# Kernel tuning notes

Hardware: AMD Instinct MI355X
Metric: run time of the kernel (lower is better)

Reference implementation:

```python
import jax, jax.numpy as jnp
import numpy as np

B, S, D_IN, H = 64, 512, 1024, 1024


def setup_inputs() -> dict:
    key = jax.random.key(0)
    ks = jax.random.split(key, 7)
    scale = 1.0 / np.sqrt(H)  # nn.LSTM init range ~ U(-1/sqrt(H), 1/sqrt(H))
    return {
        "x": jax.random.normal(ks[0], (B, S, D_IN), dtype=jnp.float32),
        "h0": jax.random.normal(ks[1], (1, B, H), dtype=jnp.float32),
        "c0": jax.random.normal(ks[2], (1, B, H), dtype=jnp.float32),
        "w_ih": jax.random.uniform(ks[3], (4 * H, D_IN), jnp.float32, -scale, scale),
        "w_hh": jax.random.uniform(ks[4], (4 * H, H), jnp.float32, -scale, scale),
        "b_ih": jax.random.uniform(ks[5], (4 * H,), jnp.float32, -scale, scale),
        "b_hh": jax.random.uniform(ks[6], (4 * H,), jnp.float32, -scale, scale),
    }


def reference(x, h0, c0, w_ih, w_hh, b_ih, b_hh):
    # Precompute the input projection for all timesteps: [B, S, 4H]
    x_proj = jnp.einsum("bsd,nd->bsn", x, w_ih)
    bias = b_ih + b_hh  # [4H]
    hdim = w_hh.shape[1]

    def step(carry, xp_t):
        h, c = carry  # [B, H] each
        gates = xp_t + h @ w_hh.T + bias  # [B, 4H], gate order i,f,g,o
        i = jax.nn.sigmoid(gates[:, 0 * hdim:1 * hdim])
        f = jax.nn.sigmoid(gates[:, 1 * hdim:2 * hdim])
        g = jnp.tanh(gates[:, 2 * hdim:3 * hdim])
        o = jax.nn.sigmoid(gates[:, 3 * hdim:4 * hdim])
        c_next = f * c + i * g
        h_next = o * jnp.tanh(c_next)
        return (h_next, c_next), None

    (h_n, _c_n), _ = jax.lax.scan(step, (h0[0], c0[0]), jnp.swapaxes(x_proj, 0, 1))
    # num_layers == 1 -> h_n_first is empty; final hidden state stacked on layer dim
    return h_n[None]  # [1, B, H]
```

## Files before the change

### kernel.cpp

```cpp
#include <hip/hip_runtime.h>

typedef short s8v __attribute__((ext_vector_type(8)));
typedef float f4v __attribute__((ext_vector_type(4)));
typedef unsigned short u16;

#define CH 128
#define NCH 4
#define NBLK 128

__device__ __forceinline__ u16 f2bf(float f) {
  unsigned u = __builtin_bit_cast(unsigned, f);
  u = (u + 0x7fffu + ((u >> 16) & 1u)) >> 16;
  return (u16)u;
}
__device__ __forceinline__ float bf2f(u16 h) {
  unsigned u = ((unsigned)h) << 16;
  return __builtin_bit_cast(float, u);
}

__global__ void k_cast(const float* __restrict__ x, const float* __restrict__ wih,
                       const float* __restrict__ whh, const float* __restrict__ bih,
                       const float* __restrict__ bhh, u16* __restrict__ xb,
                       u16* __restrict__ wihb, u16* __restrict__ whhb,
                       float* __restrict__ bias) {
  unsigned i = blockIdx.x * 256u + threadIdx.x;
  const unsigned NT = 8192u * 256u;
  for (unsigned j = i; j < 8388608u; j += NT) {
    float4 v = ((const float4*)x)[j];
    ushort4 o; o.x = f2bf(v.x); o.y = f2bf(v.y); o.z = f2bf(v.z); o.w = f2bf(v.w);
    ((ushort4*)xb)[j] = o;
  }
  if (i < 1048576u) {
    float4 v = ((const float4*)wih)[i];
    ushort4 o; o.x = f2bf(v.x); o.y = f2bf(v.y); o.z = f2bf(v.z); o.w = f2bf(v.w);
    ((ushort4*)wihb)[i] = o;
    float4 w = ((const float4*)whh)[i];
    ushort4 p; p.x = f2bf(w.x); p.y = f2bf(w.y); p.z = f2bf(w.z); p.w = f2bf(w.w);
    ((ushort4*)whhb)[i] = p;
  }
  if (i < 4096u) bias[i] = bih[i] + bhh[i];
}

__global__ __launch_bounds__(256, 2) void k_gemm(const u16* __restrict__ xb,
                                                 const u16* __restrict__ wihb,
                                                 u16* __restrict__ xpn, int s0) {
  __shared__ u16 lds[16384];
  const int t = threadIdx.x;
  const int bx = blockIdx.x;
  const int nt = bx & 31, mt = bx >> 5;
  const int lane = t & 63, w = t >> 6;
  const int wm = (w >> 1) * 64, wn = (w & 1) * 64;
  const int lr = lane & 15, lk = lane >> 4;
  f4v acc[4][4] = {};
  const size_t arow0 = (size_t)(mt * 512 + s0) * 1024;
  const size_t brow0 = (size_t)(nt * 128) * 1024;
  for (int k0 = 0; k0 < 1024; k0 += 64) {
    #pragma unroll
    for (int i = 0; i < 4; i++) {
      int f16 = i * 256 + t;
      int row = f16 >> 3;
      int colb = (f16 & 7) << 4;
      int dst = row * 128 + (colb ^ ((row & 7) << 4));
      s8v va = *(const s8v*)(xb + arow0 + (size_t)row * 1024 + k0 + (colb >> 1));
      *(s8v*)((char*)lds + dst) = va;
      s8v vb = *(const s8v*)(wihb + brow0 + (size_t)row * 1024 + k0 + (colb >> 1));
      *(s8v*)((char*)lds + 16384 + dst) = vb;
    }
    __syncthreads();
    #pragma unroll
    for (int ks = 0; ks < 2; ks++) {
      s8v af[4], bf[4];
      #pragma unroll
      for (int mi = 0; mi < 4; mi++) {
        int r = wm + mi * 16 + lr;
        int cb = (ks * 64 + lk * 16) ^ ((r & 7) << 4);
        af[mi] = *(const s8v*)((const char*)lds + r * 128 + cb);
      }
      #pragma unroll
      for (int ni = 0; ni < 4; ni++) {
        int r = wn + ni * 16 + lr;
        int cb = (ks * 64 + lk * 16) ^ ((r & 7) << 4);
        bf[ni] = *(const s8v*)((const char*)lds + 16384 + r * 128 + cb);
      }
      #pragma unroll
      for (int mi = 0; mi < 4; mi++)
        #pragma unroll
        for (int ni = 0; ni < 4; ni++)
          acc[mi][ni] = __builtin_amdgcn_mfma_f32_16x16x32_bf16(af[mi], bf[ni], acc[mi][ni], 0, 0, 0);
    }
    __syncthreads();
  }
  #pragma unroll
  for (int mi = 0; mi < 4; mi++)
    #pragma unroll
    for (int rr = 0; rr < 4; rr++) {
      int rl = wm + mi * 16 + lk * 4 + rr;
      size_t orow = ((size_t)mt * 128 + rl) * 4096;
      #pragma unroll
      for (int ni = 0; ni < 4; ni++) {
        int col = nt * 128 + wn + ni * 16 + lr;
        xpn[orow + col] = f2bf(acc[mi][ni][rr]);
      }
    }
}

__global__ void k_pack(const u16* __restrict__ xpn, u16* __restrict__ xpl) {
  const int t = threadIdx.x;
  const int bx = blockIdx.x;
  const int s = bx >> 4, ubg = bx & 15;
  const int g = t & 3, b = t >> 2;
  #pragma unroll
  for (int i = 0; i < 8; i++) {
    int ub = ubg * 8 + i;
    s8v v = *(const s8v*)(xpn + (size_t)(b * 128 + s) * 4096 + g * 1024 + ub * 8);
    *(s8v*)(xpl + (((size_t)s * 128 + ub) * 4 + g) * 512 + b * 8) = v;
  }
}

__device__ __forceinline__ void gbar2(unsigned* flags, unsigned ep) {
  __syncthreads();
  if (threadIdx.x < 64) {
    if (threadIdx.x == 0)
      __hip_atomic_store(flags + (size_t)blockIdx.x * 16, ep,
                         __ATOMIC_RELAXED, __HIP_MEMORY_SCOPE_AGENT);
    const int l = threadIdx.x;
    for (;;) {
      unsigned a = __hip_atomic_load(flags + l * 16,        __ATOMIC_RELAXED, __HIP_MEMORY_SCOPE_AGENT);
      unsigned b = __hip_atomic_load(flags + (l + 64) * 16, __ATOMIC_RELAXED, __HIP_MEMORY_SCOPE_AGENT);
      if (__all(a >= ep && b >= ep)) break;
    }
  }
  __syncthreads();
}

__global__ __launch_bounds__(256, 1) void k_rec(
    const u16* __restrict__ whhb, const u16* __restrict__ xpl,
    const float* __restrict__ bias, const float* __restrict__ h0,
    const float* __restrict__ c0, float* __restrict__ cst,
    u16* __restrict__ hbuf, float* __restrict__ out,
    unsigned* flags, int chunk) {
  const int t = threadIdx.x, bid = blockIdx.x;
  const int lane = t & 63, w = t >> 6, lr = lane & 15, lk = lane >> 4;
  s8v breg[2][32];
  #pragma unroll
  for (int nt = 0; nt < 2; nt++) {
    int grow = (lr >> 2) * 1024 + bid * 8 + nt * 4 + (lr & 3);
    const u16* wp = whhb + (size_t)grow * 1024 + lk * 8;
    #pragma unroll
    for (int ks = 0; ks < 32; ks++) breg[nt][ks] = *(const s8v*)(wp + ks * 32);
  }
  const int m = t >> 2, up = t & 3;
  const int gu0 = bid * 8 + up * 2;
  const float2 bi  = *(const float2*)(bias + gu0);
  const float2 bff = *(const float2*)(bias + 1024 + gu0);
  const float2 bgg = *(const float2*)(bias + 2048 + gu0);
  const float2 bo  = *(const float2*)(bias + 3072 + gu0);
  float2 c;
  unsigned barn = 0;
  if (chunk == 0) {
    c = *(const float2*)(c0 + m * 1024 + gu0);
    float2 hv = *(const float2*)(h0 + m * 1024 + gu0);
    unsigned hw = (unsigned)f2bf(hv.x) | ((unsigned)f2bf(hv.y) << 16);
    asm volatile("global_store_dword %0, %1, off sc0 sc1"
                 :: "v"(hbuf + m * 1024 + gu0), "v"(hw) : "memory");
    asm volatile("s_waitcnt vmcnt(0)" ::: "memory");
    barn++; gbar2(flags, barn);
  } else {
    c = *(const float2*)(cst + m * 1024 + gu0);
  }
  __shared__ float gl[2048];
  int cur = 0;
  for (int tl = 0; tl < CH; tl++) {
    const u16* xb_ = xpl + ((size_t)tl * 128 + bid) * 2048;
    unsigned xpr[4];
    #pragma unroll
    for (int g = 0; g < 4; g++)
      asm volatile("global_load_dword %0, %1, off"
                   : "=v"(xpr[g]) : "v"(xb_ + g * 512 + m * 8 + up * 2) : "memory");
    const u16* ap = hbuf + cur * 65536 + (w * 16 + lr) * 1024 + lk * 8;
    s8v af[32];
    #pragma unroll
    for (int ks = 0; ks < 32; ks++)
      asm volatile("global_load_dwordx4 %0, %1, off sc0 sc1"
                   : "=v"(af[ks]) : "v"(ap + ks * 32) : "memory");
    f4v acc0 = {0.f, 0.f, 0.f, 0.f}, acc1 = {0.f, 0.f, 0.f, 0.f};
    asm volatile("s_waitcnt vmcnt(16)" ::: "memory");
    __builtin_amdgcn_sched_barrier(0);
    #pragma unroll
    for (int ks = 0; ks < 16; ks++) {
      acc0 = __builtin_amdgcn_mfma_f32_16x16x32_bf16(af[ks], breg[0][ks], acc0, 0, 0, 0);
      acc1 = __builtin_amdgcn_mfma_f32_16x16x32_bf16(af[ks], breg[1][ks], acc1, 0, 0, 0);
    }
    asm volatile("s_waitcnt vmcnt(0)" ::: "memory");
    __builtin_amdgcn_sched_barrier(0);
    #pragma unroll
    for (int ks = 16; ks < 32; ks++) {
      acc0 = __builtin_amdgcn_mfma_f32_16x16x32_bf16(af[ks], breg[0][ks], acc0, 0, 0, 0);
      acc1 = __builtin_amdgcn_mfma_f32_16x16x32_bf16(af[ks], breg[1][ks], acc1, 0, 0, 0);
    }
    #pragma unroll
    for (int r = 0; r < 4; r++) {
      int mrow = w * 16 + lk * 4 + r;
      gl[mrow * 32 + ((lr & 3)) * 4 + (lr >> 2)] = acc0[r];
      gl[mrow * 32 + (4 + (lr & 3)) * 4 + (lr >> 2)] = acc1[r];
    }
    __syncthreads();
    float4 q0 = *(const float4*)(gl + m * 32 + up * 8);
    float4 q1 = *(const float4*)(gl + m * 32 + up * 8 + 4);
    float pi0 = q0.x + bf2f((u16)(xpr[0] & 0xffff)) + bi.x;
    float pf0 = q0.y + bf2f((u16)(xpr[1] & 0xffff)) + bff.x;
    float pg0 = q0.z + bf2f((u16)(xpr[2] & 0xffff)) + bgg.x;
    float po0 = q0.w + bf2f((u16)(xpr[3] & 0xffff)) + bo.x;
    float pi1 = q1.x + bf2f((u16)(xpr[0] >> 16)) + bi.y;
    float pf1 = q1.y + bf2f((u16)(xpr[1] >> 16)) + bff.y;
    float pg1 = q1.z + bf2f((u16)(xpr[2] >> 16)) + bgg.y;
    float po1 = q1.w + bf2f((u16)(xpr[3] >> 16)) + bo.y;
    float i0 = 1.f / (1.f + __expf(-pi0)), i1 = 1.f / (1.f + __expf(-pi1));
    float f0 = 1.f / (1.f + __expf(-pf0)), f1 = 1.f / (1.f + __expf(-pf1));
    float g0 = 1.f - 2.f / (__expf(2.f * pg0) + 1.f), g1 = 1.f - 2.f / (__expf(2.f * pg1) + 1.f);
    float o0 = 1.f / (1.f + __expf(-po0)), o1 = 1.f / (1.f + __expf(-po1));
    c.x = f0 * c.x + i0 * g0;
    c.y = f1 * c.y + i1 * g1;
    float hv0 = o0 * (1.f - 2.f / (__expf(2.f * c.x) + 1.f));
    float hv1 = o1 * (1.f - 2.f / (__expf(2.f * c.y) + 1.f));
    int nxt = cur ^ 1;
    unsigned hw = (unsigned)f2bf(hv0) | ((unsigned)f2bf(hv1) << 16);
    asm volatile("global_store_dword %0, %1, off sc0 sc1"
                 :: "v"(hbuf + nxt * 65536 + m * 1024 + gu0), "v"(hw) : "memory");
    cur = nxt;
    if (tl < CH - 1) {
      asm volatile("s_waitcnt vmcnt(0)" ::: "memory");
      barn++; gbar2(flags, barn);
    } else {
      if (chunk == NCH - 1) *(float2*)(out + m * 1024 + gu0) = make_float2(hv0, hv1);
      else *(float2*)(cst + m * 1024 + gu0) = c;
    }
  }
}

extern "C" void kernel_launch(void* const* d_in, const int* in_sizes, int n_in,
                              void* d_out, int out_size, void* d_ws, size_t ws_size,
                              hipStream_t stream) {
  const float* x   = (const float*)d_in[0];
  const float* h0  = (const float*)d_in[1];
  const float* c0  = (const float*)d_in[2];
  const float* wih = (const float*)d_in[3];
  const float* whh = (const float*)d_in[4];
  const float* bih = (const float*)d_in[5];
  const float* bhh = (const float*)d_in[6];
  float* out = (float*)d_out;
  char* ws = (char*)d_ws;
  u16* xb     = (u16*)(ws);
  u16* wihb   = (u16*)(ws + 67108864);
  u16* whhb   = (u16*)(ws + 75497472);
  float* bias = (float*)(ws + 83886080);
  u16* hbuf   = (u16*)(ws + 83902464);
  float* cst  = (float*)(ws + 84164608);
  unsigned* flags = (unsigned*)(ws + 84426752);
  u16* xpn    = (u16*)(ws + 84443136);
  u16* xpl    = (u16*)(ws + 151552000);
  (void)in_sizes; (void)n_in; (void)out_size; (void)ws_size;

  hipLaunchKernelGGL(k_cast, dim3(8192), dim3(256), 0, stream,
                     x, wih, whh, bih, bhh, xb, wihb, whhb, bias);
  for (int c = 0; c < NCH; c++) {
    hipLaunchKernelGGL(k_gemm, dim3(2048), dim3(256), 0, stream, xb, wihb, xpn, c * CH);
    hipLaunchKernelGGL(k_pack, dim3(2048), dim3(256), 0, stream, xpn, xpl);
    hipMemsetAsync(flags, 0, 16384, stream);
    hipLaunchKernelGGL(k_rec, dim3(NBLK), dim3(256), 0, stream,
                       whhb, xpl, bias, h0, c0, cst, hbuf, out, flags, c);
  }
}
```

Baseline: 3.833 ms.

## Replace block barrier with per-wave flags and fuse pack into GEMM epilogue

The GEMM epilogue now writes the input projection straight into the per-wave layout the recurrent kernel reads, so the separate pack kernel and its intermediate buffer go away. h0/c0 initialisation moves into the cast kernel. In the recurrence each wave publishes its own epoch flag and polls all 512 flags with vector loads, replacing the block-level __syncthreads plus global barrier and the per-chunk flag memset. Epochs are now monotonic across chunks. The cost is more flag traffic per poll and a scattered GEMM store pattern.

```diff
diff --git a/kernel.cpp b/kernel.cpp
--- a/kernel.cpp
+++ b/kernel.cpp
@@ -2,6 +2,7 @@
 
 typedef short s8v __attribute__((ext_vector_type(8)));
 typedef float f4v __attribute__((ext_vector_type(4)));
+typedef unsigned u32x4 __attribute__((ext_vector_type(4)));
 typedef unsigned short u16;
 
 #define CH 128
@@ -20,9 +21,11 @@
 
 __global__ void k_cast(const float* __restrict__ x, const float* __restrict__ wih,
                        const float* __restrict__ whh, const float* __restrict__ bih,
-                       const float* __restrict__ bhh, u16* __restrict__ xb,
+                       const float* __restrict__ bhh, const float* __restrict__ h0,
+                       const float* __restrict__ c0, u16* __restrict__ xb,
                        u16* __restrict__ wihb, u16* __restrict__ whhb,
-                       float* __restrict__ bias) {
+                       float* __restrict__ bias, u16* __restrict__ hbuf,
+                       float* __restrict__ cst) {
   unsigned i = blockIdx.x * 256u + threadIdx.x;
   const unsigned NT = 8192u * 256u;
   for (unsigned j = i; j < 8388608u; j += NT) {
@@ -38,12 +41,18 @@
     ushort4 p; p.x = f2bf(w.x); p.y = f2bf(w.y); p.z = f2bf(w.z); p.w = f2bf(w.w);
     ((ushort4*)whhb)[i] = p;
   }
+  if (i < 16384u) {
+    float4 v = ((const float4*)h0)[i];
+    ushort4 o; o.x = f2bf(v.x); o.y = f2bf(v.y); o.z = f2bf(v.z); o.w = f2bf(v.w);
+    ((ushort4*)hbuf)[i] = o;
+    ((float4*)cst)[i] = ((const float4*)c0)[i];
+  }
   if (i < 4096u) bias[i] = bih[i] + bhh[i];
 }
 
 __global__ __launch_bounds__(256, 2) void k_gemm(const u16* __restrict__ xb,
                                                  const u16* __restrict__ wihb,
-                                                 u16* __restrict__ xpn, int s0) {
+                                                 u16* __restrict__ xpl, int s0) {
   __shared__ u16 lds[16384];
   const int t = threadIdx.x;
   const int bx = blockIdx.x;
@@ -90,57 +99,35 @@
     }
     __syncthreads();
   }
+  int nioff[4];
+  const int bq = mt >> 4, b15 = mt & 15;
+  #pragma unroll
+  for (int ni = 0; ni < 4; ni++) {
+    int col = nt * 128 + wn + ni * 16 + lr;
+    int gate = col >> 10, u = col & 1023;
+    int gw = (u >> 3) * 4 + bq;
+    int l = (b15 << 2) | ((u >> 1) & 3);
+    nioff[ni] = gw * 512 + l * 8 + gate * 2 + (u & 1);
+  }
   #pragma unroll
   for (int mi = 0; mi < 4; mi++)
     #pragma unroll
     for (int rr = 0; rr < 4; rr++) {
-      int rl = wm + mi * 16 + lk * 4 + rr;
-      size_t orow = ((size_t)mt * 128 + rl) * 4096;
-      #pragma unroll
-      for (int ni = 0; ni < 4; ni++) {
-        int col = nt * 128 + wn + ni * 16 + lr;
-        xpn[orow + col] = f2bf(acc[mi][ni][rr]);
-      }
-    }
-}
-
-__global__ void k_pack(const u16* __restrict__ xpn, u16* __restrict__ xpl) {
-  const int t = threadIdx.x;
-  const int bx = blockIdx.x;
-  const int s = bx >> 4, ubg = bx & 15;
-  const int g = t & 3, b = t >> 2;
-  #pragma unroll
-  for (int i = 0; i < 8; i++) {
-    int ub = ubg * 8 + i;
-    s8v v = *(const s8v*)(xpn + (size_t)(b * 128 + s) * 4096 + g * 1024 + ub * 8);
-    *(s8v*)(xpl + (((size_t)s * 128 + ub) * 4 + g) * 512 + b * 8) = v;
-  }
-}
-
-__device__ __forceinline__ void gbar2(unsigned* flags, unsigned ep) {
-  __syncthreads();
-  if (threadIdx.x < 64) {
-    if (threadIdx.x == 0)
-      __hip_atomic_store(flags + (size_t)blockIdx.x * 16, ep,
-                         __ATOMIC_RELAXED, __HIP_MEMORY_SCOPE_AGENT);
-    const int l = threadIdx.x;
-    for (;;) {
-      unsigned a = __hip_atomic_load(flags + l * 16,        __ATOMIC_RELAXED, __HIP_MEMORY_SCOPE_AGENT);
-      unsigned b = __hip_atomic_load(flags + (l + 64) * 16, __ATOMIC_RELAXED, __HIP_MEMORY_SCOPE_AGENT);
-      if (__all(a >= ep && b >= ep)) break;
-    }
-  }
-  __syncthreads();
+      int tloc = wm + mi * 16 + lk * 4 + rr;
+      u16* dst = xpl + (size_t)tloc * 262144;
+      #pragma unroll
+      for (int ni = 0; ni < 4; ni++) dst[nioff[ni]] = f2bf(acc[mi][ni][rr]);
+    }
 }
 
 __global__ __launch_bounds__(256, 1) void k_rec(
     const u16* __restrict__ whhb, const u16* __restrict__ xpl,
-    const float* __restrict__ bias, const float* __restrict__ h0,
-    const float* __restrict__ c0, float* __restrict__ cst,
+    const float* __restrict__ bias, float* __restrict__ cst,
     u16* __restrict__ hbuf, float* __restrict__ out,
     unsigned* flags, int chunk) {
   const int t = threadIdx.x, bid = blockIdx.x;
   const int lane = t & 63, w = t >> 6, lr = lane & 15, lk = lane >> 4;
+  const int gwid = bid * 4 + w;
   s8v breg[2][32];
   #pragma unroll
   for (int nt = 0; nt < 2; nt++) {
@@ -149,34 +136,33 @@
     #pragma unroll
     for (int ks = 0; ks < 32; ks++) breg[nt][ks] = *(const s8v*)(wp + ks * 32);
   }
-  const int m = t >> 2, up = t & 3;
-  const int gu0 = bid * 8 + up * 2;
-  const float2 bi  = *(const float2*)(bias + gu0);
-  const float2 bff = *(const float2*)(bias + 1024 + gu0);
-  const float2 bgg = *(const float2*)(bias + 2048 + gu0);
-  const float2 bo  = *(const float2*)(bias + 3072 + gu0);
-  float2 c;
-  unsigned barn = 0;
-  if (chunk == 0) {
-    c = *(const float2*)(c0 + m * 1024 + gu0);
-    float2 hv = *(const float2*)(h0 + m * 1024 + gu0);
-    unsigned hw = (unsigned)f2bf(hv.x) | ((unsigned)f2bf(hv.y) << 16);
-    asm volatile("global_store_dword %0, %1, off sc0 sc1"
-                 :: "v"(hbuf + m * 1024 + gu0), "v"(hw) : "memory");
-    asm volatile("s_waitcnt vmcnt(0)" ::: "memory");
-    barn++; gbar2(flags, barn);
-  } else {
-    c = *(const float2*)(cst + m * 1024 + gu0);
-  }
-  __shared__ float gl[2048];
+  const int me = w * 16 + (lane >> 2);
+  const int u0 = bid * 8 + (lane & 3) * 2;
+  const float2 bi  = *(const float2*)(bias + u0);
+  const float2 bff = *(const float2*)(bias + 1024 + u0);
+  const float2 bgg = *(const float2*)(bias + 2048 + u0);
+  const float2 bo  = *(const float2*)(bias + 3072 + u0);
+  float2 c = *(const float2*)(cst + me * 1024 + u0);
+  __shared__ float gl[4][16 * 36];
+  float* glw = gl[w];
+  const unsigned epb = (unsigned)(chunk * CH);
   int cur = 0;
   for (int tl = 0; tl < CH; tl++) {
-    const u16* xb_ = xpl + ((size_t)tl * 128 + bid) * 2048;
-    unsigned xpr[4];
-    #pragma unroll
-    for (int g = 0; g < 4; g++)
-      asm volatile("global_load_dword %0, %1, off"
-                   : "=v"(xpr[g]) : "v"(xb_ + g * 512 + m * 8 + up * 2) : "memory");
+    s8v xq;
+    asm volatile("global_load_dwordx4 %0, %1, off"
+                 : "=v"(xq) : "v"(xpl + (size_t)tl * 262144 + gwid * 512 + lane * 8) : "memory");
+    if (tl > 0) {
+      unsigned ep = epb + (unsigned)tl;
+      const unsigned* fp = flags + lane * 8;
+      for (;;) {
+        u32x4 fa, fb;
+        asm volatile("global_load_dwordx4 %0, %1, off sc0 sc1" : "=v"(fa) : "v"(fp) : "memory");
+        asm volatile("global_load_dwordx4 %0, %1, off sc0 sc1" : "=v"(fb) : "v"(fp + 4) : "memory");
+        asm volatile("s_waitcnt vmcnt(0)" ::: "memory");
+        if (__all(fa.x >= ep && fa.y >= ep && fa.z >= ep && fa.w >= ep &&
+                  fb.x >= ep && fb.y >= ep && fb.z >= ep && fb.w >= ep)) break;
+      }
+    }
     const u16* ap = hbuf + cur * 65536 + (w * 16 + lr) * 1024 + lk * 8;
     s8v af[32];
     #pragma unroll
@@ -200,21 +186,22 @@
     }
     #pragma unroll
     for (int r = 0; r < 4; r++) {
-      int mrow = w * 16 + lk * 4 + r;
-      gl[mrow * 32 + ((lr & 3)) * 4 + (lr >> 2)] = acc0[r];
-      gl[mrow * 32 + (4 + (lr & 3)) * 4 + (lr >> 2)] = acc1[r];
-    }
-    __syncthreads();
-    float4 q0 = *(const float4*)(gl + m * 32 + up * 8);
-    float4 q1 = *(const float4*)(gl + m * 32 + up * 8 + 4);
-    float pi0 = q0.x + bf2f((u16)(xpr[0] & 0xffff)) + bi.x;
-    float pf0 = q0.y + bf2f((u16)(xpr[1] & 0xffff)) + bff.x;
-    float pg0 = q0.z + bf2f((u16)(xpr[2] & 0xffff)) + bgg.x;
-    float po0 = q0.w + bf2f((u16)(xpr[3] & 0xffff)) + bo.x;
-    float pi1 = q1.x + bf2f((u16)(xpr[0] >> 16)) + bi.y;
-    float pf1 = q1.y + bf2f((u16)(xpr[1] >> 16)) + bff.y;
-    float pg1 = q1.z + bf2f((u16)(xpr[2] >> 16)) + bgg.y;
-    float po1 = q1.w + bf2f((u16)(xpr[3] >> 16)) + bo.y;
+      int mrow = lk * 4 + r;
+      glw[mrow * 36 + (lr & 3) * 4 + (lr >> 2)] = acc0[r];
+      glw[mrow * 36 + 16 + (lr & 3) * 4 + (lr >> 2)] = acc1[r];
+    }
+    asm volatile("s_waitcnt lgkmcnt(0)" ::: "memory");
+    __builtin_amdgcn_sched_barrier(0);
+    float4 q0 = *(const float4*)(glw + (lane >> 2) * 36 + (lane & 3) * 8);
+    float4 q1 = *(const float4*)(glw + (lane >> 2) * 36 + (lane & 3) * 8 + 4);
+    float pi0 = q0.x + bf2f((u16)xq[0]) + bi.x;
+    float pi1 = q1.x + bf2f((u16)xq[1]) + bi.y;
+    float pf0 = q0.y + bf2f((u16)xq[2]) + bff.x;
+    float pf1 = q1.y + bf2f((u16)xq[3]) + bff.y;
+    float pg0 = q0.z + bf2f((u16)xq[4]) + bgg.x;
+    float pg1 = q1.z + bf2f((u16)xq[5]) + bgg.y;
+    float po0 = q0.w + bf2f((u16)xq[6]) + bo.x;
+    float po1 = q1.w + bf2f((u16)xq[7]) + bo.y;
     float i0 = 1.f / (1.f + __expf(-pi0)), i1 = 1.f / (1.f + __expf(-pi1));
     float f0 = 1.f / (1.f + __expf(-pf0)), f1 = 1.f / (1.f + __expf(-pf1));
     float g0 = 1.f - 2.f / (__expf(2.f * pg0) + 1.f), g1 = 1.f - 2.f / (__expf(2.f * pg1) + 1.f);
@@ -226,14 +213,18 @@
     int nxt = cur ^ 1;
     unsigned hw = (unsigned)f2bf(hv0) | ((unsigned)f2bf(hv1) << 16);
     asm volatile("global_store_dword %0, %1, off sc0 sc1"
-                 :: "v"(hbuf + nxt * 65536 + m * 1024 + gu0), "v"(hw) : "memory");
+                 :: "v"(hbuf + nxt * 65536 + me * 1024 + u0), "v"(hw) : "memory");
     cur = nxt;
     if (tl < CH - 1) {
       asm volatile("s_waitcnt vmcnt(0)" ::: "memory");
-      barn++; gbar2(flags, barn);
+      if (lane == 0) {
+        unsigned fv = epb + (unsigned)tl + 1u;
+        asm volatile("global_store_dword %0, %1, off sc0 sc1"
+                     :: "v"(flags + gwid), "v"(fv) : "memory");
+      }
     } else {
-      if (chunk == NCH - 1) *(float2*)(out + m * 1024 + gu0) = make_float2(hv0, hv1);
-      else *(float2*)(cst + m * 1024 + gu0) = c;
+      if (chunk == NCH - 1) *(float2*)(out + me * 1024 + u0) = make_float2(hv0, hv1);
+      else *(float2*)(cst + me * 1024 + u0) = c;
     }
   }
 }
@@ -257,17 +248,15 @@
   u16* hbuf   = (u16*)(ws + 83902464);
   float* cst  = (float*)(ws + 84164608);
   unsigned* flags = (unsigned*)(ws + 84426752);
-  u16* xpn    = (u16*)(ws + 84443136);
-  u16* xpl    = (u16*)(ws + 151552000);
+  u16* xpl    = (u16*)(ws + 84428800);
   (void)in_sizes; (void)n_in; (void)out_size; (void)ws_size;
 
+  hipMemsetAsync(flags, 0, 2048, stream);
   hipLaunchKernelGGL(k_cast, dim3(8192), dim3(256), 0, stream,
-                     x, wih, whh, bih, bhh, xb, wihb, whhb, bias);
+                     x, wih, whh, bih, bhh, h0, c0, xb, wihb, whhb, bias, hbuf, cst);
   for (int c = 0; c < NCH; c++) {
-    hipLaunchKernelGGL(k_gemm, dim3(2048), dim3(256), 0, stream, xb, wihb, xpn, c * CH);
-    hipLaunchKernelGGL(k_pack, dim3(2048), dim3(256), 0, stream, xpn, xpl);
-    hipMemsetAsync(flags, 0, 16384, stream);
+    hipLaunchKernelGGL(k_gemm, dim3(2048), dim3(256), 0, stream, xb, wihb, xpl, c * CH);
     hipLaunchKernelGGL(k_rec, dim3(NBLK), dim3(256), 0, stream,
-                       whhb, xpl, bias, h0, c0, cst, hbuf, out, flags, c);
-  }
-}
+                       whhb, xpl, bias, cst, hbuf, out, flags, c);
+  }
+}
```

Result: slower. 5.963 ms (+55.5%).
